# Performance work log

Measured on AMD Instinct MI355X. Metric: run time of the kernel, lower is better.

## Reference

```python
import jax, jax.numpy as jnp
import numpy as np

SCORE_THRESHOLD = 0.35
TARGET_CLASS_ID = 0.0
R = 4_194_304  # number of candidate detections (rois)


def setup_inputs() -> dict:
    key = jax.random.key(0)
    k1, k2, k3 = jax.random.split(key, 3)
    class_ids = jax.random.randint(k1, (R,), 0, 4).astype(jnp.float32)
    boxes = jax.random.uniform(k2, (R, 4), dtype=jnp.float32)
    scores = jax.random.uniform(k3, (R,), dtype=jnp.float32)
    detections = jnp.concatenate([class_ids[:, None], boxes, scores[:, None]], axis=1)[None]  # [1, R, 6]
    return {"detections": detections}


def _compact(data, mask):
    # Stable stream compaction with fixed output shape: valid rows moved to the
    # front (original order preserved), invalid tail zero-padded.
    # data: [R, D] float, mask: [R] bool  ->  ([R, D], n_valid)
    order = jnp.argsort(jnp.logical_not(mask), stable=True)  # valid (False-key) first
    sel = jnp.take(data, order, axis=0)
    n = jnp.sum(mask.astype(jnp.int32))
    keep = (jnp.arange(data.shape[0]) < n)[:, None]
    return jnp.where(keep, sel, jnp.zeros((), data.dtype)), n


def reference(detections):
    # detections: [1, R, 6] = [class_id, x1, y1, x2, y2, score]
    d = detections[0]
    class_ids = d[:, 0]
    scores = d[:, 5]
    valid = (class_ids == TARGET_CLASS_ID) & (scores >= SCORE_THRESHOLD)
    valid_full = scores >= SCORE_THRESHOLD

    sel, n = _compact(d, valid)
    # rois: zero class stub + xyxy (score dropped), [1, R, 5]; padded rows are all-zero
    rois = jnp.concatenate([jnp.zeros((d.shape[0], 1), d.dtype), sel[:, 1:5]], axis=1)[None]

    rois_full, n_full = _compact(d, valid_full)
    rois_full = rois_full[None]  # [1, R, 6]

    return rois, rois_full, n, n_full
```

## Files before the change

kernel.cpp:

```cpp
#include <hip/hip_runtime.h>

typedef unsigned int uint32;
typedef unsigned long long uint64;

#define BLOCK 256
#define IPT 16
#define CHUNK (BLOCK * IPT)
#define RPI 512
#define SCORE_THR 0.35f

__global__ void count_kernel(const float* __restrict__ det,
                             uint32* __restrict__ c0, uint32* __restrict__ c1,
                             int R) {
    int tid = threadIdx.x;
    int wave = tid >> 6, lane = tid & 63;
    long long base = (long long)blockIdx.x * CHUNK;
    uint32 cnt0 = 0, cnt1 = 0;

    if (base + CHUNK <= R) {
        const float4* d4 = (const float4*)det + base * 6 / 4;
        for (int it = 0; it < IPT / 2; ++it) {
            const float4* p = d4 + (long long)it * (BLOCK * 3) + 3 * tid;
            float4 f0 = p[0], f1 = p[1], f2 = p[2];
            bool mA1 = (f1.y >= SCORE_THR);
            bool mA0 = mA1 && (f0.x == 0.0f);
            bool mB1 = (f2.w >= SCORE_THR);
            bool mB0 = mB1 && (f1.z == 0.0f);
            cnt1 += (mA1 ? 1u : 0u) + (mB1 ? 1u : 0u);
            cnt0 += (mA0 ? 1u : 0u) + (mB0 ? 1u : 0u);
        }
    } else {
        for (int i = 0; i < IPT; ++i) {
            long long row = base + (long long)i * BLOCK + tid;
            if (row < R) {
                float c = det[row * 6 + 0];
                float s = det[row * 6 + 5];
                bool m1 = (s >= SCORE_THR);
                bool m0 = m1 && (c == 0.0f);
                cnt1 += m1 ? 1u : 0u;
                cnt0 += m0 ? 1u : 0u;
            }
        }
    }

    for (int off = 32; off > 0; off >>= 1) {
        cnt0 += __shfl_down(cnt0, off, 64);
        cnt1 += __shfl_down(cnt1, off, 64);
    }
    __shared__ uint32 ra[4], rb[4];
    if (lane == 0) { ra[wave] = cnt0; rb[wave] = cnt1; }
    __syncthreads();
    if (tid == 0) {
        c0[blockIdx.x] = ra[0] + ra[1] + ra[2] + ra[3];
        c1[blockIdx.x] = rb[0] + rb[1] + rb[2] + rb[3];
    }
}

__device__ inline void zero_region(float* p, long long n,
                                   long long gtid, long long gstride) {
    if (n <= 0) return;
    long long head = ((4 - (((size_t)p >> 2) & 3)) & 3);
    if (head > n) head = n;
    if (gtid < head) p[gtid] = 0.0f;
    long long n4 = (n - head) >> 2;
    float4* b = (float4*)(p + head);
    float4 z4 = make_float4(0.f, 0.f, 0.f, 0.f);
    for (long long k = gtid; k < n4; k += gstride) b[k] = z4;
    long long done = head + (n4 << 2);
    long long rem = n - done;
    if (gtid < rem) p[done + gtid] = 0.0f;
}

__global__ void scatter_zero_kernel(const float* __restrict__ det,
                                    float* __restrict__ rois, float* __restrict__ roisf,
                                    const uint32* __restrict__ c0, const uint32* __restrict__ c1,
                                    float* __restrict__ out_n,
                                    int R, int NB) {
    int tid = threadIdx.x;
    int wave = tid >> 6, lane = tid & 63;
    int bid = blockIdx.x;

    uint32 pre0 = 0, pre1 = 0, tot0 = 0, tot1 = 0;
    for (int j = tid; j < NB; j += BLOCK) {
        uint32 a = c0[j], b = c1[j];
        tot0 += a; tot1 += b;
        if (j < bid) { pre0 += a; pre1 += b; }
    }
    for (int off = 32; off > 0; off >>= 1) {
        pre0 += __shfl_down(pre0, off, 64);
        pre1 += __shfl_down(pre1, off, 64);
        tot0 += __shfl_down(tot0, off, 64);
        tot1 += __shfl_down(tot1, off, 64);
    }
    __shared__ uint32 lp0[4], lp1[4], lt0[4], lt1[4];
    if (lane == 0) { lp0[wave] = pre0; lp1[wave] = pre1; lt0[wave] = tot0; lt1[wave] = tot1; }
    __syncthreads();
    pre0 = lp0[0] + lp0[1] + lp0[2] + lp0[3];
    pre1 = lp1[0] + lp1[1] + lp1[2] + lp1[3];
    tot0 = lt0[0] + lt0[1] + lt0[2] + lt0[3];
    tot1 = lt1[0] + lt1[1] + lt1[2] + lt1[3];

    if (bid == 0 && tid == 0) {
        out_n[0] = (float)tot0;
        out_n[1] = (float)tot1;
    }

    __shared__ uint32 wc0[2][4], wc1[2][4];
    __shared__ float st0[2][RPI * 5];
    __shared__ float st1[2][RPI * 6];
    uint32 run0 = pre0, run1 = pre1;
    long long base = (long long)bid * CHUNK;
    uint64 ltmask = (1ull << lane) - 1ull;

    if (base + CHUNK <= R) {
        const float4* d4 = (const float4*)det + base * 6 / 4;
        for (int it = 0; it < IPT / 2; ++it) {
            int buf = it & 1;
            const float4* p = d4 + (long long)it * (BLOCK * 3) + 3 * tid;
            float4 f0 = p[0], f1 = p[1], f2 = p[2];
            bool mA1 = (f1.y >= SCORE_THR);
            bool mA0 = mA1 && (f0.x == 0.0f);
            bool mB1 = (f2.w >= SCORE_THR);
            bool mB0 = mB1 && (f1.z == 0.0f);

            uint64 bA0 = __ballot(mA0), bA1 = __ballot(mA1);
            uint64 bB0 = __ballot(mB0), bB1 = __ballot(mB1);

            if (lane == 0) {
                wc0[buf][wave] = (uint32)(__popcll(bA0) + __popcll(bB0));
                wc1[buf][wave] = (uint32)(__popcll(bA1) + __popcll(bB1));
            }
            __syncthreads();
            uint32 wp0 = 0, wp1 = 0, bt0 = 0, bt1 = 0;
            for (int w = 0; w < 4; ++w) {
                uint32 a = wc0[buf][w], b = wc1[buf][w];
                bt0 += a; bt1 += b;
                if (w < wave) { wp0 += a; wp1 += b; }
            }
            uint32 lA0 = wp0 + (uint32)(__popcll(bA0 & ltmask) + __popcll(bB0 & ltmask));
            uint32 lB0 = lA0 + (mA0 ? 1u : 0u);
            uint32 lA1 = wp1 + (uint32)(__popcll(bA1 & ltmask) + __popcll(bB1 & ltmask));
            uint32 lB1 = lA1 + (mA1 ? 1u : 0u);

            if (mA0) {
                float* s = &st0[buf][lA0 * 5];
                s[0] = 0.0f; s[1] = f0.y; s[2] = f0.z; s[3] = f0.w; s[4] = f1.x;
            }
            if (mB0) {
                float* s = &st0[buf][lB0 * 5];
                s[0] = 0.0f; s[1] = f1.w; s[2] = f2.x; s[3] = f2.y; s[4] = f2.z;
            }
            if (mA1) {
                float* s = &st1[buf][lA1 * 6];
                s[0] = f0.x; s[1] = f0.y; s[2] = f0.z; s[3] = f0.w; s[4] = f1.x; s[5] = f1.y;
            }
            if (mB1) {
                float* s = &st1[buf][lB1 * 6];
                s[0] = f1.z; s[1] = f1.w; s[2] = f2.x; s[3] = f2.y; s[4] = f2.z; s[5] = f2.w;
            }
            __syncthreads();

            uint32 N0 = bt0 * 5, N1 = bt1 * 6;
            float* g0 = rois + (long long)run0 * 5;
            float* g1 = roisf + (long long)run1 * 6;
            for (uint32 j = tid; j < N0; j += BLOCK) g0[j] = st0[buf][j];
            for (uint32 j = tid; j < N1; j += BLOCK) g1[j] = st1[buf][j];
            run0 += bt0; run1 += bt1;
        }
    } else {
        for (int i = 0; i < IPT; ++i) {
            long long row = base + (long long)i * BLOCK + tid;
            bool m0 = false, m1 = false;
            float d0 = 0, d1 = 0, d2 = 0, d3 = 0, d4v = 0, d5 = 0;
            if (row < R) {
                const float* pp = det + row * 6;
                d0 = pp[0]; d1 = pp[1]; d2 = pp[2]; d3 = pp[3]; d4v = pp[4]; d5 = pp[5];
                m1 = (d5 >= SCORE_THR);
                m0 = m1 && (d0 == 0.0f);
            }
            uint64 b0 = __ballot(m0), b1 = __ballot(m1);
            int buf = i & 1;
            if (lane == 0) {
                wc0[buf][wave] = (uint32)__popcll(b0);
                wc1[buf][wave] = (uint32)__popcll(b1);
            }
            __syncthreads();
            uint32 wp0 = 0, wp1 = 0, bt0 = 0, bt1 = 0;
            for (int w = 0; w < 4; ++w) {
                uint32 a = wc0[buf][w], b = wc1[buf][w];
                bt0 += a; bt1 += b;
                if (w < wave) { wp0 += a; wp1 += b; }
            }
            if (m0) {
                uint32 pos = run0 + wp0 + (uint32)__popcll(b0 & ltmask);
                float* q = rois + (long long)pos * 5;
                q[0] = 0.0f; q[1] = d1; q[2] = d2; q[3] = d3; q[4] = d4v;
            }
            if (m1) {
                uint32 pos = run1 + wp1 + (uint32)__popcll(b1 & ltmask);
                float* q = roisf + (long long)pos * 6;
                q[0] = d0; q[1] = d1; q[2] = d2; q[3] = d3; q[4] = d4v; q[5] = d5;
            }
            run0 += bt0; run1 += bt1;
            __syncthreads();
        }
    }

    long long gtid = (long long)bid * BLOCK + tid;
    long long gstride = (long long)NB * BLOCK;
    zero_region(rois + (long long)tot0 * 5, (long long)(R - (long long)tot0) * 5,
                gtid, gstride);
    zero_region(roisf + (long long)tot1 * 6, (long long)(R - (long long)tot1) * 6,
                gtid, gstride);
}

extern "C" void kernel_launch(void* const* d_in, const int* in_sizes, int n_in,
                              void* d_out, int out_size, void* d_ws, size_t ws_size,
                              hipStream_t stream) {
    const float* det = (const float*)d_in[0];
    float* out = (float*)d_out;
    int R = in_sizes[0] / 6;
    int NB = (R + CHUNK - 1) / CHUNK;

    uint32* ws = (uint32*)d_ws;
    uint32* c0 = ws;
    uint32* c1 = ws + NB;

    float* rois  = out;
    float* roisf = out + (long long)R * 5;
    float* nout  = out + (long long)R * 11;

    count_kernel<<<NB, BLOCK, 0, stream>>>(det, c0, c1, R);
    scatter_zero_kernel<<<NB, BLOCK, 0, stream>>>(det, rois, roisf, c0, c1, nout, R, NB);
}
```

Measured before the change: 286.9 us.

## Fuse count and scatter into single-pass decoupled look-back compaction kernel

Replaces the separate count and scatter kernels with one kernel that takes a dynamic block ticket, publishes per-block aggregates, and resolves its exclusive prefix through a decoupled look-back over packed 64-bit state words. Each block also zeroes only its own slice of the padded tail, replacing the grid-strided global zeroing. This removes a second launch and one of the two reads of the input, at the cost of a memset, spin-waiting on predecessors, and atomic traffic on the state array. The chunk input is read twice inside the block (count, then scatter) and will likely be served from cache.

```diff
diff --git a/kernel.cpp b/kernel.cpp
--- a/kernel.cpp
+++ b/kernel.cpp
@@ -9,16 +9,54 @@
 #define RPI 512
 #define SCORE_THR 0.35f
 
-__global__ void count_kernel(const float* __restrict__ det,
-                             uint32* __restrict__ c0, uint32* __restrict__ c1,
-                             int R) {
+#define FLAG_AGG 1ull
+#define FLAG_PRE 2ull
+
+__device__ inline uint64 pack_state(uint64 flag, uint32 v0, uint32 v1) {
+    return (flag << 62) | ((uint64)v1 << 23) | (uint64)v0;
+}
+
+__device__ inline void zero_span(float* p, long long lo, long long hi, int tid) {
+    long long n = hi - lo;
+    if (n <= 0) return;
+    float* q = p + lo;
+    long long head = (4 - (((size_t)q >> 2) & 3)) & 3;
+    if (head > n) head = n;
+    if (tid < head) q[tid] = 0.0f;
+    long long n4 = (n - head) >> 2;
+    float4* b4 = (float4*)(q + head);
+    float4 z = make_float4(0.f, 0.f, 0.f, 0.f);
+    for (long long k = tid; k < n4; k += BLOCK) b4[k] = z;
+    long long done = head + (n4 << 2);
+    if (tid < n - done) q[done + tid] = 0.0f;
+}
+
+__global__ void __launch_bounds__(BLOCK)
+fused_kernel(const float* __restrict__ det,
+             float* __restrict__ rois, float* __restrict__ roisf,
+             uint64* state, uint32* ticket,
+             float* __restrict__ out_n, int R, int NB) {
     int tid = threadIdx.x;
     int wave = tid >> 6, lane = tid & 63;
-    long long base = (long long)blockIdx.x * CHUNK;
+
+    __shared__ uint32 sh_bid;
+    __shared__ uint32 sh_e[2];
+    __shared__ uint32 red0[4], red1[4];
+    __shared__ uint32 wc0[2][4], wc1[2][4];
+    __shared__ float st0[2][RPI * 5];
+    __shared__ float st1[2][RPI * 6];
+
+    if (tid == 0) sh_bid = atomicAdd(ticket, 1u);
+    __syncthreads();
+    int bid = (int)sh_bid;
+
+    long long base = (long long)bid * CHUNK;
+    int rows = (int)min((long long)CHUNK, (long long)R - base);
+    bool full = (rows == CHUNK);
+    const float4* d4 = (const float4*)(det + base * 6);
+
     uint32 cnt0 = 0, cnt1 = 0;
-
-    if (base + CHUNK <= R) {
-        const float4* d4 = (const float4*)det + base * 6 / 4;
+    if (full) {
         for (int it = 0; it < IPT / 2; ++it) {
             const float4* p = d4 + (long long)it * (BLOCK * 3) + 3 * tid;
             float4 f0 = p[0], f1 = p[1], f2 = p[2];
@@ -31,89 +69,70 @@
         }
     } else {
         for (int i = 0; i < IPT; ++i) {
-            long long row = base + (long long)i * BLOCK + tid;
-            if (row < R) {
-                float c = det[row * 6 + 0];
-                float s = det[row * 6 + 5];
-                bool m1 = (s >= SCORE_THR);
-                bool m0 = m1 && (c == 0.0f);
+            int r = i * BLOCK + tid;
+            if (r < rows) {
+                const float* pp = det + (base + r) * 6;
+                bool m1 = (pp[5] >= SCORE_THR);
+                bool m0 = m1 && (pp[0] == 0.0f);
                 cnt1 += m1 ? 1u : 0u;
                 cnt0 += m0 ? 1u : 0u;
             }
         }
     }
-
-    for (int off = 32; off > 0; off >>= 1) {
+    for (int off = 32; off; off >>= 1) {
         cnt0 += __shfl_down(cnt0, off, 64);
         cnt1 += __shfl_down(cnt1, off, 64);
     }
-    __shared__ uint32 ra[4], rb[4];
-    if (lane == 0) { ra[wave] = cnt0; rb[wave] = cnt1; }
+    if (lane == 0) { red0[wave] = cnt0; red1[wave] = cnt1; }
     __syncthreads();
-    if (tid == 0) {
-        c0[blockIdx.x] = ra[0] + ra[1] + ra[2] + ra[3];
-        c1[blockIdx.x] = rb[0] + rb[1] + rb[2] + rb[3];
-    }
-}
-
-__device__ inline void zero_region(float* p, long long n,
-                                   long long gtid, long long gstride) {
-    if (n <= 0) return;
-    long long head = ((4 - (((size_t)p >> 2) & 3)) & 3);
-    if (head > n) head = n;
-    if (gtid < head) p[gtid] = 0.0f;
-    long long n4 = (n - head) >> 2;
-    float4* b = (float4*)(p + head);
-    float4 z4 = make_float4(0.f, 0.f, 0.f, 0.f);
-    for (long long k = gtid; k < n4; k += gstride) b[k] = z4;
-    long long done = head + (n4 << 2);
-    long long rem = n - done;
-    if (gtid < rem) p[done + gtid] = 0.0f;
-}
-
-__global__ void scatter_zero_kernel(const float* __restrict__ det,
-                                    float* __restrict__ rois, float* __restrict__ roisf,
-                                    const uint32* __restrict__ c0, const uint32* __restrict__ c1,
-                                    float* __restrict__ out_n,
-                                    int R, int NB) {
-    int tid = threadIdx.x;
-    int wave = tid >> 6, lane = tid & 63;
-    int bid = blockIdx.x;
-
-    uint32 pre0 = 0, pre1 = 0, tot0 = 0, tot1 = 0;
-    for (int j = tid; j < NB; j += BLOCK) {
-        uint32 a = c0[j], b = c1[j];
-        tot0 += a; tot1 += b;
-        if (j < bid) { pre0 += a; pre1 += b; }
-    }
-    for (int off = 32; off > 0; off >>= 1) {
-        pre0 += __shfl_down(pre0, off, 64);
-        pre1 += __shfl_down(pre1, off, 64);
-        tot0 += __shfl_down(tot0, off, 64);
-        tot1 += __shfl_down(tot1, off, 64);
-    }
-    __shared__ uint32 lp0[4], lp1[4], lt0[4], lt1[4];
-    if (lane == 0) { lp0[wave] = pre0; lp1[wave] = pre1; lt0[wave] = tot0; lt1[wave] = tot1; }
+    uint32 a0 = red0[0] + red0[1] + red0[2] + red0[3];
+    uint32 a1 = red1[0] + red1[1] + red1[2] + red1[3];
+
+    if (tid == 0 && bid > 0)
+        atomicExch(&state[bid], pack_state(FLAG_AGG, a0, a1));
+
+    if (wave == 0) {
+        uint32 e0 = 0, e1 = 0;
+        if (bid > 0) {
+            int wb = bid;
+            while (true) {
+                int idx = wb - 1 - lane;
+                uint64 s = (idx >= 0) ? atomicAdd(&state[idx], 0ull)
+                                      : pack_state(FLAG_PRE, 0u, 0u);
+                uint32 flag = (uint32)(s >> 62);
+                uint64 pre_mask  = __ballot(flag == 2u);
+                uint64 nrdy_mask = __ballot(flag == 0u);
+                int pl = pre_mask ? (int)(__ffsll(pre_mask) - 1) : 64;
+                uint64 below = (pl >= 64) ? ~0ull : ((1ull << pl) - 1ull);
+                if ((nrdy_mask & below) == 0ull) {
+                    uint32 v0 = (uint32)(s & 0x7FFFFFu);
+                    uint32 v1 = (uint32)((s >> 23) & 0x7FFFFFu);
+                    if (lane > pl) { v0 = 0; v1 = 0; }
+                    for (int off = 32; off; off >>= 1) {
+                        v0 += __shfl_xor(v0, off, 64);
+                        v1 += __shfl_xor(v1, off, 64);
+                    }
+                    e0 += v0; e1 += v1;
+                    if (pl < 64) break;
+                    wb -= 64;
+                } else {
+                    __builtin_amdgcn_s_sleep(1);
+                }
+            }
+        }
+        if (lane == 0) {
+            uint32 i0 = e0 + a0, i1 = e1 + a1;
+            atomicExch(&state[bid], pack_state(FLAG_PRE, i0, i1));
+            sh_e[0] = e0; sh_e[1] = e1;
+            if (bid == NB - 1) { out_n[0] = (float)i0; out_n[1] = (float)i1; }
+        }
+    }
     __syncthreads();
-    pre0 = lp0[0] + lp0[1] + lp0[2] + lp0[3];
-    pre1 = lp1[0] + lp1[1] + lp1[2] + lp1[3];
-    tot0 = lt0[0] + lt0[1] + lt0[2] + lt0[3];
-    tot1 = lt1[0] + lt1[1] + lt1[2] + lt1[3];
-
-    if (bid == 0 && tid == 0) {
-        out_n[0] = (float)tot0;
-        out_n[1] = (float)tot1;
-    }
-
-    __shared__ uint32 wc0[2][4], wc1[2][4];
-    __shared__ float st0[2][RPI * 5];
-    __shared__ float st1[2][RPI * 6];
-    uint32 run0 = pre0, run1 = pre1;
-    long long base = (long long)bid * CHUNK;
+    uint32 e0s = sh_e[0], e1s = sh_e[1];
+    uint32 run0 = e0s, run1 = e1s;
     uint64 ltmask = (1ull << lane) - 1ull;
 
-    if (base + CHUNK <= R) {
-        const float4* d4 = (const float4*)det + base * 6 / 4;
+    if (full) {
         for (int it = 0; it < IPT / 2; ++it) {
             int buf = it & 1;
             const float4* p = d4 + (long long)it * (BLOCK * 3) + 3 * tid;
@@ -169,11 +188,11 @@
         }
     } else {
         for (int i = 0; i < IPT; ++i) {
-            long long row = base + (long long)i * BLOCK + tid;
+            int r = i * BLOCK + tid;
             bool m0 = false, m1 = false;
             float d0 = 0, d1 = 0, d2 = 0, d3 = 0, d4v = 0, d5 = 0;
-            if (row < R) {
-                const float* pp = det + row * 6;
+            if (r < rows) {
+                const float* pp = det + (base + r) * 6;
                 d0 = pp[0]; d1 = pp[1]; d2 = pp[2]; d3 = pp[3]; d4v = pp[4]; d5 = pp[5];
                 m1 = (d5 >= SCORE_THR);
                 m0 = m1 && (d0 == 0.0f);
@@ -206,12 +225,18 @@
         }
     }
 
-    long long gtid = (long long)bid * BLOCK + tid;
-    long long gstride = (long long)NB * BLOCK;
-    zero_region(rois + (long long)tot0 * 5, (long long)(R - (long long)tot0) * 5,
-                gtid, gstride);
-    zero_region(roisf + (long long)tot1 * 6, (long long)(R - (long long)tot1) * 6,
-                gtid, gstride);
+    {
+        long long D = base - (long long)e0s;
+        long long hi = (long long)R - D;
+        long long lo = hi - ((long long)rows - (long long)a0);
+        zero_span(rois, lo * 5, hi * 5, tid);
+    }
+    {
+        long long D = base - (long long)e1s;
+        long long hi = (long long)R - D;
+        long long lo = hi - ((long long)rows - (long long)a1);
+        zero_span(roisf, lo * 6, hi * 6, tid);
+    }
 }
 
 extern "C" void kernel_launch(void* const* d_in, const int* in_sizes, int n_in,
@@ -222,14 +247,14 @@
     int R = in_sizes[0] / 6;
     int NB = (R + CHUNK - 1) / CHUNK;
 
-    uint32* ws = (uint32*)d_ws;
-    uint32* c0 = ws;
-    uint32* c1 = ws + NB;
+    uint64* state = (uint64*)d_ws;
+    uint32* ticket = (uint32*)(state + NB);
 
     float* rois  = out;
     float* roisf = out + (long long)R * 5;
     float* nout  = out + (long long)R * 11;
 
-    count_kernel<<<NB, BLOCK, 0, stream>>>(det, c0, c1, R);
-    scatter_zero_kernel<<<NB, BLOCK, 0, stream>>>(det, rois, roisf, c0, c1, nout, R, NB);
-}
+    hipMemsetAsync(d_ws, 0, (size_t)(NB + 1) * 8, stream);
+    fused_kernel<<<NB, BLOCK, 0, stream>>>(det, rois, roisf, state, ticket,
+                                           nout, R, NB);
+}
```

Result: no change. 289.9 us (+1.1%).
